# Performance work log

Hardware: AMD Instinct MI355X
Metric: run time of the kernel (lower is better)

The kernel has to match this reference:

```python
import jax, jax.numpy as jnp
import numpy as np

BN_EPS = 1e-5

def _bn_relu(x, gamma, beta):
    # x: [B, C, N]; BatchNorm1d in training mode: stats over (B, N) per channel
    mean = jnp.mean(x, axis=(0, 2), keepdims=True)
    var = jnp.var(x, axis=(0, 2), keepdims=True)
    xn = (x - mean) * jax.lax.rsqrt(var + BN_EPS)
    return jax.nn.relu(xn * gamma[None, :, None] + beta[None, :, None])


def setup_inputs() -> dict:
    key = jax.random.key(0)
    ks = jax.random.split(key, 8)
    B, N, S, D1, D2 = 16, 4096, 1024, 64, 256
    C_in, H = D1 + D2, 256  # mlp_list = [320, 256, 256]
    inp = {
        "xyz1": jax.random.normal(ks[0], (B, 3, N), jnp.float32),
        "xyz2": jax.random.normal(ks[1], (B, 3, S), jnp.float32),
        "points1": jax.random.normal(ks[2], (B, D1, N), jnp.float32),
        "points2": jax.random.normal(ks[3], (B, D2, S), jnp.float32),
        # 1x1 Conv1d weights of the SeqLinear pointNet MLP
        "W1": jax.random.normal(ks[4], (H, C_in), jnp.float32) / np.sqrt(C_in),
        "b1": jnp.zeros((H,), jnp.float32),
        "g1": jnp.ones((H,), jnp.float32),
        "bt1": jnp.zeros((H,), jnp.float32),
        "W2": jax.random.normal(ks[5], (H, H), jnp.float32) / np.sqrt(H),
        "b2": jnp.zeros((H,), jnp.float32),
        "g2": jnp.ones((H,), jnp.float32),
        "bt2": jnp.zeros((H,), jnp.float32),
    }
    return inp


def reference(xyz1, xyz2, points1, points2, W1, b1, g1, bt1, W2, b2, g2, bt2):
    x1 = jnp.transpose(xyz1, (0, 2, 1))   # [B, N, 3]
    x2 = jnp.transpose(xyz2, (0, 2, 1))   # [B, S, 3]
    p2 = jnp.transpose(points2, (0, 2, 1))  # [B, S, D2]
    B, N, _ = x1.shape

    # square_distance: ||x1||^2 + ||x2||^2 - 2 x1.x2  -> [B, N, S]
    dists = (jnp.sum(x1 * x1, axis=-1, keepdims=True)
             + jnp.sum(x2 * x2, axis=-1)[:, None, :]
             - 2.0 * jnp.einsum('bnc,bsc->bns', x1, x2))

    # 3 nearest neighbors (smallest distances)
    neg_d3, idx = jax.lax.top_k(-dists, 3)   # [B, N, 3]
    d3 = -neg_d3
    recip = 1.0 / (d3 + 1e-8)
    weight = recip / jnp.sum(recip, axis=2, keepdims=True)  # [B, N, 3]

    # gather neighbor features: [B, N, 3, D2]
    gathered = jax.vmap(lambda p, i: p[i])(p2, idx)
    interp = jnp.sum(gathered * weight[..., None], axis=2)  # [B, N, D2]

    new_points = jnp.concatenate([jnp.transpose(points1, (0, 2, 1)), interp], axis=-1)
    x = jnp.transpose(new_points, (0, 2, 1))  # [B, 320, N]

    # pointNet MLP: conv1x1 -> BN -> ReLU, twice
    h = jnp.einsum('oc,bcn->bon', W1, x) + b1[None, :, None]
    h = _bn_relu(h, g1, bt1)
    h = jnp.einsum('oc,bcn->bon', W2, h) + b2[None, :, None]
    h = _bn_relu(h, g2, bt2)
    return h
```

## Files before the change

kernel.cpp:

```cpp
#include <hip/hip_runtime.h>
#include <cstddef>

#define B_   16
#define N_   4096
#define S_   1024
#define D1_  64
#define D2_  256
#define CIN_ 320
#define H_   256
#define CH_  8
#define SC_  (S_ / CH_)
#define P_   (B_ * (N_ / 128))

using short8 = __attribute__((ext_vector_type(8))) short;
using f32x4  = __attribute__((ext_vector_type(4))) float;

typedef const __attribute__((address_space(1))) unsigned g1u32;
typedef __attribute__((address_space(3))) unsigned l3u32;

__device__ __forceinline__ void gl_lds16(const void* g, void* l) {
  __builtin_amdgcn_global_load_lds((g1u32*)g, (l3u32*)l, 16, 0, 0);
}

__device__ __forceinline__ float relu_f(float v) { return fmaxf(v, 0.0f); }

__device__ __forceinline__ ushort f2bf(float f) {
  unsigned u = __builtin_bit_cast(unsigned, f);
  u += 0x7fffu + ((u >> 16) & 1u);
  return (ushort)(u >> 16);
}
__device__ __forceinline__ float bf2f(ushort u) {
  return __builtin_bit_cast(float, (unsigned)u << 16);
}

__global__ __launch_bounds__(256) void prep(
    const float* __restrict__ points2, const float* __restrict__ W1,
    const float* __restrict__ W2, ushort* __restrict__ p2tb,
    ushort* __restrict__ W1b, ushort* __restrict__ W2b) {
  int g = blockIdx.x, t = threadIdx.x;
  if (g < 4096) {
    __shared__ float tile[32][33];
    int z = g >> 8, rem = g & 255;
    int c0 = (rem & 31) * 32;
    int r0 = (rem >> 5) * 32;
    const float* in = points2 + (size_t)z * D2_ * S_;
    ushort* out = p2tb + (size_t)z * S_ * D2_;
    int tx = t & 31, ty = t >> 5;
#pragma unroll
    for (int j = 0; j < 4; ++j) {
      int r = r0 + ty + j * 8;
      tile[ty + j * 8][tx] = in[(size_t)r * S_ + c0 + tx];
    }
    __syncthreads();
#pragma unroll
    for (int j = 0; j < 4; ++j) {
      int c = c0 + ty + j * 8;
      out[(size_t)c * D2_ + r0 + tx] = f2bf(tile[tx][ty + j * 8]);
    }
  } else {
    int g2 = g - 4096;
    const float* src = (g2 < 40) ? W1 : W2;
    ushort* dst = (g2 < 40) ? W1b : W2b;
    int base = ((g2 < 40) ? g2 : g2 - 40) * 2048 + t * 8;
    float4 a = *(const float4*)&src[base];
    float4 b = *(const float4*)&src[base + 4];
    short8 r;
    r[0] = (short)f2bf(a.x); r[1] = (short)f2bf(a.y);
    r[2] = (short)f2bf(a.z); r[3] = (short)f2bf(a.w);
    r[4] = (short)f2bf(b.x); r[5] = (short)f2bf(b.y);
    r[6] = (short)f2bf(b.z); r[7] = (short)f2bf(b.w);
    *(short8*)&dst[base] = r;
  }
}

__global__ __launch_bounds__(256) void knn3_part(
    const float* __restrict__ xyz1, const float* __restrict__ xyz2,
    float* __restrict__ pd, int* __restrict__ pi) {
  __shared__ float4 P[SC_];
  int b = blockIdx.z, ch = blockIdx.y;
  int n = blockIdx.x * 256 + threadIdx.x;
  const float* x2b = xyz2 + (size_t)b * 3 * S_ + ch * SC_;
  if (threadIdx.x < SC_) {
    int i = threadIdx.x;
    float x = x2b[i], y = x2b[S_ + i], z = x2b[2 * S_ + i];
    P[i] = make_float4(-2.f * x, -2.f * y, -2.f * z, x * x + y * y + z * z);
  }
  __syncthreads();

  const float* x1b = xyz1 + (size_t)b * 3 * N_;
  float px = x1b[n], py = x1b[N_ + n], pz = x1b[2 * N_ + n];
  float sq1 = px * px + py * py + pz * pz;

  float d0 = 1e30f, d1 = 1e30f, d2 = 1e30f;
  int i0 = 0, i1 = 0, i2 = 0;
#pragma unroll 4
  for (int s = 0; s < SC_; ++s) {
    float4 p = P[s];
    float d = fmaf(px, p.x, fmaf(py, p.y, fmaf(pz, p.z, p.w)));
    int gi = ch * SC_ + s;
    if (d < d2) {
      if (d < d1) {
        if (d < d0) { d2 = d1; i2 = i1; d1 = d0; i1 = i0; d0 = d; i0 = gi; }
        else        { d2 = d1; i2 = i1; d1 = d;  i1 = gi; }
      } else        { d2 = d;  i2 = gi; }
    }
  }
  size_t base = (((size_t)b * N_ + n) * CH_ + ch) * 3;
  pd[base] = d0 + sq1; pd[base + 1] = d1 + sq1; pd[base + 2] = d2 + sq1;
  pi[base] = i0; pi[base + 1] = i1; pi[base + 2] = i2;
}

__global__ __launch_bounds__(256) void build_fused(
    const float* __restrict__ points1,
    const ushort* __restrict__ p2tb,
    const float* __restrict__ pd, const int* __restrict__ pi,
    ushort* __restrict__ xt) {
  __shared__ int   lidx[16][3];
  __shared__ float lw[16][3];
  __shared__ ushort p1t[16][72];
  int g = blockIdx.x, t = threadIdx.x;
  int b = g & 15;
  int p0 = (g >> 4) * 16;

  if (t < 16) {
    size_t pb = (size_t)b * N_ + p0 + t;
    const float* pdp = pd + pb * 24;
    const int*   pip = pi + pb * 24;
    float d0 = 1e30f, d1 = 1e30f, d2 = 1e30f;
    int i0 = 0, i1 = 0, i2 = 0;
#pragma unroll
    for (int k = 0; k < 24; ++k) {
      float d = pdp[k];
      int gi = pip[k];
      if (d < d2) {
        if (d < d1) {
          if (d < d0) { d2 = d1; i2 = i1; d1 = d0; i1 = i0; d0 = d; i0 = gi; }
          else        { d2 = d1; i2 = i1; d1 = d;  i1 = gi; }
        } else        { d2 = d;  i2 = gi; }
      }
    }
    float r0 = 1.0f / (d0 + 1e-8f);
    float r1 = 1.0f / (d1 + 1e-8f);
    float r2 = 1.0f / (d2 + 1e-8f);
    float rs = 1.0f / (r0 + r1 + r2);
    lidx[t][0] = i0; lidx[t][1] = i1; lidx[t][2] = i2;
    lw[t][0] = r0 * rs; lw[t][1] = r1 * rs; lw[t][2] = r2 * rs;
  }

  {
    int c = t >> 2, q4 = t & 3;
    float4 v = *(const float4*)&points1[((size_t)b * D1_ + c) * N_ + p0 + q4 * 4];
    p1t[q4 * 4 + 0][c] = f2bf(v.x);
    p1t[q4 * 4 + 1][c] = f2bf(v.y);
    p1t[q4 * 4 + 2][c] = f2bf(v.z);
    p1t[q4 * 4 + 3][c] = f2bf(v.w);
  }
  __syncthreads();

  int pl = t >> 4, q = t & 15;
  size_t pb = (size_t)b * N_ + p0 + pl;
  int i0 = lidx[pl][0], i1 = lidx[pl][1], i2 = lidx[pl][2];
  float w0 = lw[pl][0], w1 = lw[pl][1], w2 = lw[pl][2];
  const ushort* R0 = p2tb + ((size_t)b * S_ + i0) * D2_;
  const ushort* R1 = p2tb + ((size_t)b * S_ + i1) * D2_;
  const ushort* R2 = p2tb + ((size_t)b * S_ + i2) * D2_;
  ushort* o = xt + pb * CIN_;

  if (q < 8)
    *(short8*)(o + q * 8) = *(const short8*)&p1t[pl][q * 8];

#pragma unroll
  for (int it = 0; it < 2; ++it) {
    int c = it * 16 + q;
    short8 a = *(const short8*)&R0[c * 8];
    short8 d = *(const short8*)&R1[c * 8];
    short8 e = *(const short8*)&R2[c * 8];
    short8 r;
#pragma unroll
    for (int u = 0; u < 8; ++u) {
      float v = w0 * bf2f((ushort)a[u]) + w1 * bf2f((ushort)d[u]) +
                w2 * bf2f((ushort)e[u]);
      r[u] = (short)f2bf(v);
    }
    *(short8*)(o + D1_ + c * 8) = r;
  }
}

template <int K, bool BNIN>
__global__ __launch_bounds__(256) void gemm_pipe(
    const ushort* __restrict__ Wb, const ushort* __restrict__ Xt,
    const float* __restrict__ bias, const float* __restrict__ scin,
    const float* __restrict__ shin, ushort* __restrict__ Yt,
    float* __restrict__ ps1, float* __restrict__ ps2) {
  constexpr int NT = K / 64;
  __shared__ union SM {
    struct { ushort A[2][128][64]; ushort Bt[2][128][64]; } st;
    struct { ushort C[128][132]; float S1[128][33]; float S2[128][33]; } ep;
  } sm;
  __shared__ float scs_l[H_], shs_l[H_];

  int b  = blockIdx.z;
  int n0 = blockIdx.x * 128;
  int m0 = blockIdx.y * 128;
  int tid = threadIdx.x;
  int lane = tid & 63, wid = tid >> 6;
  int wm = (wid >> 1) * 64, wn = (wid & 1) * 64;
  int lr = lane & 15, hi = lane >> 4;
  size_t bn0 = (size_t)b * N_ + n0;

  if (BNIN) {
    for (int i = tid; i < K; i += 256) { scs_l[i] = scin[i]; shs_l[i] = shin[i]; }
  }

  const char* Agb = (const char*)(Wb + (size_t)m0 * K);
  const char* Bgb = (const char*)(Xt + bn0 * K);
  const size_t rowB = (size_t)K * 2;

  size_t gsrc[4];
  int    ldst[4];
#pragma unroll
  for (int r = 0; r < 4; ++r) {
    int m = (wid * 4 + r) * 64 + lane;
    int row = m >> 3;
    int c = ((m & 7) - row) & 7;
    gsrc[r] = (size_t)row * rowB + (size_t)c * 16;
    ldst[r] = m * 16;
  }

  auto stage = [&](int buf, int kc) {
    char* bA = (char*)sm.st.A[buf];
    char* bB = (char*)sm.st.Bt[buf];
    size_t kb = (size_t)kc * 128;
#pragma unroll
    for (int r = 0; r < 4; ++r) {
      gl_lds16(Agb + gsrc[r] + kb, bA + ldst[r]);
      gl_lds16(Bgb + gsrc[r] + kb, bB + ldst[r]);
    }
  };

  f32x4 acc[4][4] = {};

  stage(0, 0);
  __syncthreads();

  int cur = 0;
  for (int t = 0; t < NT; ++t) {
    if (t + 1 < NT) stage(cur ^ 1, t + 1);
#pragma unroll
    for (int ks = 0; ks < 2; ++ks) {
      short8 af[4], bv[4];
#pragma unroll
      for (int i = 0; i < 4; ++i) {
        int rA = wm + i * 16 + lr;
        int rB = wn + i * 16 + lr;
        int sA = (rA + ks * 4 + hi) & 7;
        int sB = (rB + ks * 4 + hi) & 7;
        af[i] = *(const short8*)&sm.st.A[cur][rA][sA * 8];
        bv[i] = *(const short8*)&sm.st.Bt[cur][rB][sB * 8];
      }
      if (BNIN) {
        int kb = t * 64 + ks * 32 + hi * 8;
        f32x4 sa = *(const f32x4*)&scs_l[kb];
        f32x4 sb = *(const f32x4*)&scs_l[kb + 4];
        f32x4 ha = *(const f32x4*)&shs_l[kb];
        f32x4 hb = *(const f32x4*)&shs_l[kb + 4];
#pragma unroll
        for (int i = 0; i < 4; ++i) {
          short8 pk;
#pragma unroll
          for (int e = 0; e < 4; ++e) {
            pk[e]     = (short)f2bf(relu_f(bf2f((ushort)bv[i][e]) * sa[e] + ha[e]));
            pk[e + 4] = (short)f2bf(relu_f(bf2f((ushort)bv[i][e + 4]) * sb[e] + hb[e]));
          }
          bv[i] = pk;
        }
      }
#pragma unroll
      for (int mf = 0; mf < 4; ++mf)
#pragma unroll
        for (int nf = 0; nf < 4; ++nf)
          acc[mf][nf] = __builtin_amdgcn_mfma_f32_16x16x32_bf16(
              af[mf], bv[nf], acc[mf][nf], 0, 0, 0);
    }
    __syncthreads();
    cur ^= 1;
  }

  float sum1[4][4] = {}, sum2[4][4] = {};
#pragma unroll
  for (int mf = 0; mf < 4; ++mf) {
#pragma unroll
    for (int nf = 0; nf < 4; ++nf) {
      int n = wn + nf * 16 + lr;
      ushort4 u;
#pragma unroll
      for (int j = 0; j < 4; ++j) {
        float v = acc[mf][nf][j] + bias[m0 + wm + mf * 16 + hi * 4 + j];
        sum1[mf][j] += v;
        sum2[mf][j] += v * v;
        ((ushort*)&u)[j] = f2bf(v);
      }
      *(ushort4*)&sm.ep.C[n][wm + mf * 16 + hi * 4] = u;
    }
  }
  __syncthreads();
  {
    int rown = tid >> 4, q = tid & 15;
#pragma unroll
    for (int p = 0; p < 8; ++p) {
      int n = p * 16 + rown;
      short8 val = *(const short8*)&sm.ep.C[n][q * 8];
      *(short8*)&Yt[(bn0 + n) * H_ + m0 + q * 8] = val;
    }
  }
  int col = (wid & 1) * 16 + lr;
#pragma unroll
  for (int mf = 0; mf < 4; ++mf)
#pragma unroll
    for (int j = 0; j < 4; ++j) {
      int c = wm + mf * 16 + hi * 4 + j;
      sm.ep.S1[c][col] = sum1[mf][j];
      sm.ep.S2[c][col] = sum2[mf][j];
    }
  __syncthreads();
  int pidx = b * gridDim.x + blockIdx.x;
  int c = tid & 127;
  float s = 0.f;
  if (tid < 128) {
#pragma unroll
    for (int k = 0; k < 32; ++k) s += sm.ep.S1[c][k];
    ps1[(size_t)pidx * H_ + m0 + c] = s;
  } else {
#pragma unroll
    for (int k = 0; k < 32; ++k) s += sm.ep.S2[c][k];
    ps2[(size_t)pidx * H_ + m0 + c] = s;
  }
}

__global__ __launch_bounds__(256) void bn_stats_fin(
    const float* __restrict__ ps1, const float* __restrict__ ps2,
    const float* __restrict__ gamma, const float* __restrict__ beta,
    float* __restrict__ sc, float* __restrict__ sh) {
  int c = blockIdx.x, t = threadIdx.x;
  float s1 = ps1[(size_t)t * H_ + c] + ps1[(size_t)(t + 256) * H_ + c];
  float s2 = ps2[(size_t)t * H_ + c] + ps2[(size_t)(t + 256) * H_ + c];
  __shared__ float S1[256], S2[256];
  S1[t] = s1; S2[t] = s2;
  __syncthreads();
  for (int off = 128; off > 0; off >>= 1) {
    if (t < off) { S1[t] += S1[t + off]; S2[t] += S2[t + off]; }
    __syncthreads();
  }
  if (t == 0) {
    const float inv = 1.0f / (float)(B_ * N_);
    float mean = S1[0] * inv;
    float var  = S2[0] * inv - mean * mean;
    float g    = gamma[c] * rsqrtf(var + 1e-5f);
    sc[c] = g;
    sh[c] = beta[c] - mean * g;
  }
}

__global__ __launch_bounds__(256) void bn_out_t(
    const ushort* __restrict__ Hb, const float* __restrict__ sc,
    const float* __restrict__ sh, float* __restrict__ out) {
  __shared__ float tile[32][132];
  int b = blockIdx.z;
  int n0 = blockIdx.x * 32, m0 = blockIdx.y * 128;
  int t = threadIdx.x;
  int m8 = (t & 15) * 8;
  f32x4 sa = *(const f32x4*)&sc[m0 + m8];
  f32x4 sb = *(const f32x4*)&sc[m0 + m8 + 4];
  f32x4 ha = *(const f32x4*)&sh[m0 + m8];
  f32x4 hb = *(const f32x4*)&sh[m0 + m8 + 4];
  size_t bn0 = (size_t)b * N_ + n0;
#pragma unroll
  for (int pass = 0; pass < 2; ++pass) {
    int n = pass * 16 + (t >> 4);
    short8 v = *(const short8*)&Hb[(bn0 + n) * H_ + m0 + m8];
#pragma unroll
    for (int e = 0; e < 4; ++e) {
      tile[n][m8 + e]     = relu_f(bf2f((ushort)v[e]) * sa[e] + ha[e]);
      tile[n][m8 + 4 + e] = relu_f(bf2f((ushort)v[e + 4]) * sb[e] + hb[e]);
    }
  }
  __syncthreads();
  int m = t >> 1, nh = (t & 1) * 16;
  float* orow = out + ((size_t)b * H_ + m0 + m) * N_ + n0 + nh;
#pragma unroll
  for (int j = 0; j < 4; ++j) {
    float4 v;
    v.x = tile[nh + j * 4 + 0][m];
    v.y = tile[nh + j * 4 + 1][m];
    v.z = tile[nh + j * 4 + 2][m];
    v.w = tile[nh + j * 4 + 3][m];
    *(float4*)&orow[j * 4] = v;
  }
}

extern "C" void kernel_launch(void* const* d_in, const int* in_sizes, int n_in,
                              void* d_out, int out_size, void* d_ws,
                              size_t ws_size, hipStream_t stream) {
  const float* xyz1    = (const float*)d_in[0];
  const float* xyz2    = (const float*)d_in[1];
  const float* points1 = (const float*)d_in[2];
  const float* points2 = (const float*)d_in[3];
  const float* W1  = (const float*)d_in[4];
  const float* b1  = (const float*)d_in[5];
  const float* g1  = (const float*)d_in[6];
  const float* bt1 = (const float*)d_in[7];
  const float* W2  = (const float*)d_in[8];
  const float* b2  = (const float*)d_in[9];
  const float* g2  = (const float*)d_in[10];
  const float* bt2 = (const float*)d_in[11];
  float* out = (float*)d_out;
  char* cur = (char*)d_ws;
  auto alloc = [&](size_t bytes) { char* p = cur; cur += (bytes + 255) & ~255ull; return p; };

  ushort* p2tb = (ushort*)alloc((size_t)B_ * S_ * D2_ * 2);
  float*  pd   = (float*)alloc((size_t)B_ * N_ * CH_ * 3 * 4);
  int*    pi   = (int*)alloc((size_t)B_ * N_ * CH_ * 3 * 4);
  ushort* W1b  = (ushort*)alloc((size_t)H_ * CIN_ * 2);
  ushort* W2b  = (ushort*)alloc((size_t)H_ * H_ * 2);
  ushort* xct  = (ushort*)alloc((size_t)B_ * N_ * CIN_ * 2);
  ushort* h1t  = (ushort*)alloc((size_t)B_ * N_ * H_ * 2);
  float*  ps1  = (float*)alloc((size_t)P_ * H_ * 4);
  float*  ps2  = (float*)alloc((size_t)P_ * H_ * 4);
  float*  sc1  = (float*)alloc(H_ * 4);
  float*  sh1  = (float*)alloc(H_ * 4);
  float*  sc2  = (float*)alloc(H_ * 4);
  float*  sh2  = (float*)alloc(H_ * 4);
  ushort* h2b  = xct;

  prep<<<4096 + 40 + 32, 256, 0, stream>>>(points2, W1, W2, p2tb, W1b, W2b);

  knn3_part<<<dim3(N_ / 256, CH_, B_), 256, 0, stream>>>(xyz1, xyz2, pd, pi);

  build_fused<<<B_ * N_ / 16, 256, 0, stream>>>(points1, p2tb, pd, pi, xct);

  gemm_pipe<CIN_, false><<<dim3(N_ / 128, H_ / 128, B_), 256, 0, stream>>>(
      W1b, xct, b1, nullptr, nullptr, h1t, ps1, ps2);
  bn_stats_fin<<<H_, 256, 0, stream>>>(ps1, ps2, g1, bt1, sc1, sh1);

  gemm_pipe<H_, true><<<dim3(N_ / 128, H_ / 128, B_), 256, 0, stream>>>(
      W2b, h1t, b2, sc1, sh1, h2b, ps1, ps2);
  bn_stats_fin<<<H_, 256, 0, stream>>>(ps1, ps2, g2, bt2, sc2, sh2);

  bn_out_t<<<dim3(N_ / 32, H_ / 128, B_), 256, 0, stream>>>(h2b, sc2, sh2, out);
}
```

Before: 159.5 us.

## Fuse feature interpolation and concat into the first GEMM's B-tile construction

Removes the separate build kernel that wrote the concatenated bf16 input matrix to global memory. The first GEMM now merges the partial KNN results, computes the interpolation weights, loads points1 directly into the first B tile, and builds each later 64-channel B tile from gathered points2 rows while the MFMAs run. This saves a write and re-read of the large intermediate plus one launch. In exchange the interpolation is recomputed once per M-block (two blocks cover H), the B-tile gathers are synchronous per stage, and a separate h2 buffer is now allocated.

New measurement: 166.5 us. +4.4%, slower.

```diff
diff --git a/kernel.cpp b/kernel.cpp
--- a/kernel.cpp
+++ b/kernel.cpp
@@ -110,20 +110,69 @@
   pi[base] = i0; pi[base + 1] = i1; pi[base + 2] = i2;
 }
 
-__global__ __launch_bounds__(256) void build_fused(
+__global__ __launch_bounds__(256) void gemm_build(
+    const ushort* __restrict__ Wb,
     const float* __restrict__ points1,
     const ushort* __restrict__ p2tb,
     const float* __restrict__ pd, const int* __restrict__ pi,
-    ushort* __restrict__ xt) {
-  __shared__ int   lidx[16][3];
-  __shared__ float lw[16][3];
-  __shared__ ushort p1t[16][72];
-  int g = blockIdx.x, t = threadIdx.x;
-  int b = g & 15;
-  int p0 = (g >> 4) * 16;
-
-  if (t < 16) {
-    size_t pb = (size_t)b * N_ + p0 + t;
+    const float* __restrict__ bias, ushort* __restrict__ Yt,
+    float* __restrict__ ps1, float* __restrict__ ps2) {
+  constexpr int K = CIN_, NT = K / 64;
+  __shared__ union SM {
+    struct { ushort A[2][128][64]; ushort Bt[2][128][64]; } st;
+    struct { ushort C[128][132]; float S1[128][33]; float S2[128][33]; } ep;
+  } sm;
+  __shared__ float lw[128][3];
+  __shared__ int   lidx[128][3];
+
+  int b  = blockIdx.z;
+  int n0 = blockIdx.x * 128;
+  int m0 = blockIdx.y * 128;
+  int tid = threadIdx.x;
+  int lane = tid & 63, wid = tid >> 6;
+  int wm = (wid >> 1) * 64, wn = (wid & 1) * 64;
+  int lr = lane & 15, hi = lane >> 4;
+  size_t bn0 = (size_t)b * N_ + n0;
+
+  const char* Agb = (const char*)(Wb + (size_t)m0 * K);
+  const size_t rowB = (size_t)K * 2;
+
+  size_t gsrcA[4];
+  int    ldstA[4];
+#pragma unroll
+  for (int r = 0; r < 4; ++r) {
+    int m = (wid * 4 + r) * 64 + lane;
+    int row = m >> 3;
+    int c = ((m & 7) - row) & 7;
+    gsrcA[r] = (size_t)row * rowB + (size_t)c * 16;
+    ldstA[r] = m * 16;
+  }
+  auto stageA = [&](int buf, int kc) {
+    char* bA = (char*)sm.st.A[buf];
+    size_t kb = (size_t)kc * 128;
+#pragma unroll
+    for (int r = 0; r < 4; ++r)
+      gl_lds16(Agb + gsrcA[r] + kb, bA + ldstA[r]);
+  };
+
+  stageA(0, 0);
+  {
+    int c = tid & 63, nq = tid >> 6;
+    const float* s1 = points1 + ((size_t)b * D1_ + c) * N_ + n0 + nq * 32;
+    int cc0 = c >> 3, ce = c & 7;
+#pragma unroll
+    for (int j = 0; j < 8; ++j) {
+      float4 v = *(const float4*)&s1[j * 4];
+      const float* vp = (const float*)&v;
+#pragma unroll
+      for (int e = 0; e < 4; ++e) {
+        int r = nq * 32 + j * 4 + e;
+        sm.st.Bt[0][r][(((r + cc0) & 7) << 3) + ce] = f2bf(vp[e]);
+      }
+    }
+  }
+  if (tid < 128) {
+    size_t pb = bn0 + tid;
     const float* pdp = pd + pb * 24;
     const int*   pip = pi + pb * 24;
     float d0 = 1e30f, d1 = 1e30f, d2 = 1e30f;
@@ -143,50 +192,117 @@
     float r1 = 1.0f / (d1 + 1e-8f);
     float r2 = 1.0f / (d2 + 1e-8f);
     float rs = 1.0f / (r0 + r1 + r2);
-    lidx[t][0] = i0; lidx[t][1] = i1; lidx[t][2] = i2;
-    lw[t][0] = r0 * rs; lw[t][1] = r1 * rs; lw[t][2] = r2 * rs;
-  }
-
+    lidx[tid][0] = i0; lidx[tid][1] = i1; lidx[tid][2] = i2;
+    lw[tid][0] = r0 * rs; lw[tid][1] = r1 * rs; lw[tid][2] = r2 * rs;
+  }
+  __syncthreads();
+
+  int pt = tid >> 1, hh = (tid & 1) * 4;
+  float w0 = lw[pt][0], w1 = lw[pt][1], w2 = lw[pt][2];
+  const ushort* R0 = p2tb + ((size_t)b * S_ + lidx[pt][0]) * D2_;
+  const ushort* R1 = p2tb + ((size_t)b * S_ + lidx[pt][1]) * D2_;
+  const ushort* R2 = p2tb + ((size_t)b * S_ + lidx[pt][2]) * D2_;
+
+  auto buildB = [&](int buf, int kc) {
+    int pc0 = (kc - 1) * 64;
+#pragma unroll
+    for (int c2 = 0; c2 < 4; ++c2) {
+      int cc = hh + c2;
+      int pch = pc0 + cc * 8;
+      short8 a = *(const short8*)&R0[pch];
+      short8 d = *(const short8*)&R1[pch];
+      short8 e = *(const short8*)&R2[pch];
+      short8 r;
+#pragma unroll
+      for (int u = 0; u < 8; ++u) {
+        float v = w0 * bf2f((ushort)a[u]) + w1 * bf2f((ushort)d[u]) +
+                  w2 * bf2f((ushort)e[u]);
+        r[u] = (short)f2bf(v);
+      }
+      *(short8*)&sm.st.Bt[buf][pt][((pt + cc) & 7) * 8] = r;
+    }
+  };
+
+  f32x4 acc[4][4] = {};
+  int cur = 0;
+  for (int t = 0; t < NT; ++t) {
+    if (t + 1 < NT) stageA(cur ^ 1, t + 1);
+#pragma unroll
+    for (int ks = 0; ks < 2; ++ks) {
+      short8 af[4], bv[4];
+#pragma unroll
+      for (int i = 0; i < 4; ++i) {
+        int rA = wm + i * 16 + lr;
+        int rB = wn + i * 16 + lr;
+        int sA = (rA + ks * 4 + hi) & 7;
+        int sB = (rB + ks * 4 + hi) & 7;
+        af[i] = *(const short8*)&sm.st.A[cur][rA][sA * 8];
+        bv[i] = *(const short8*)&sm.st.Bt[cur][rB][sB * 8];
+      }
+#pragma unroll
+      for (int mf = 0; mf < 4; ++mf)
+#pragma unroll
+        for (int nf = 0; nf < 4; ++nf)
+          acc[mf][nf] = __builtin_amdgcn_mfma_f32_16x16x32_bf16(
+              af[mf], bv[nf], acc[mf][nf], 0, 0, 0);
+    }
+    if (t + 1 < NT) buildB(cur ^ 1, t + 1);
+    __syncthreads();
+    cur ^= 1;
+  }
+
+  float sum1[4][4] = {}, sum2[4][4] = {};
+#pragma unroll
+  for (int mf = 0; mf < 4; ++mf) {
+#pragma unroll
+    for (int nf = 0; nf < 4; ++nf) {
+      int n = wn + nf * 16 + lr;
+      ushort4 u;
+#pragma unroll
+      for (int j = 0; j < 4; ++j) {
+        float v = acc[mf][nf][j] + bias[m0 + wm + mf * 16 + hi * 4 + j];
+        sum1[mf][j] += v;
+        sum2[mf][j] += v * v;
+        ((ushort*)&u)[j] = f2bf(v);
+      }
+      *(ushort4*)&sm.ep.C[n][wm + mf * 16 + hi * 4] = u;
+    }
+  }
+  __syncthreads();
   {
-    int c = t >> 2, q4 = t & 3;
-    float4 v = *(const float4*)&points1[((size_t)b * D1_ + c) * N_ + p0 + q4 * 4];
-    p1t[q4 * 4 + 0][c] = f2bf(v.x);
-    p1t[q4 * 4 + 1][c] = f2bf(v.y);
-    p1t[q4 * 4 + 2][c] = f2bf(v.z);
-    p1t[q4 * 4 + 3][c] = f2bf(v.w);
-  }
-  __syncthreads();
-
-  int pl = t >> 4, q = t & 15;
-  size_t pb = (size_t)b * N_ + p0 + pl;
-  int i0 = lidx[pl][0], i1 = lidx[pl][1], i2 = lidx[pl][2];
-  float w0 = lw[pl][0], w1 = lw[pl][1], w2 = lw[pl][2];
-  const ushort* R0 = p2tb + ((size_t)b * S_ + i0) * D2_;
-  const ushort* R1 = p2tb + ((size_t)b * S_ + i1) * D2_;
-  const ushort* R2 = p2tb + ((size_t)b * S_ + i2) * D2_;
-  ushort* o = xt + pb * CIN_;
-
-  if (q < 8)
-    *(short8*)(o + q * 8) = *(const short8*)&p1t[pl][q * 8];
-
-#pragma unroll
-  for (int it = 0; it < 2; ++it) {
-    int c = it * 16 + q;
-    short8 a = *(const short8*)&R0[c * 8];
-    short8 d = *(const short8*)&R1[c * 8];
-    short8 e = *(const short8*)&R2[c * 8];
-    short8 r;
-#pragma unroll
-    for (int u = 0; u < 8; ++u) {
-      float v = w0 * bf2f((ushort)a[u]) + w1 * bf2f((ushort)d[u]) +
-                w2 * bf2f((ushort)e[u]);
-      r[u] = (short)f2bf(v);
-    }
-    *(short8*)(o + D1_ + c * 8) = r;
-  }
-}
-
-template <int K, bool BNIN>
+    int rown = tid >> 4, q = tid & 15;
+#pragma unroll
+    for (int p = 0; p < 8; ++p) {
+      int n = p * 16 + rown;
+      short8 val = *(const short8*)&sm.ep.C[n][q * 8];
+      *(short8*)&Yt[(bn0 + n) * H_ + m0 + q * 8] = val;
+    }
+  }
+  int col = (wid & 1) * 16 + lr;
+#pragma unroll
+  for (int mf = 0; mf < 4; ++mf)
+#pragma unroll
+    for (int j = 0; j < 4; ++j) {
+      int c = wm + mf * 16 + hi * 4 + j;
+      sm.ep.S1[c][col] = sum1[mf][j];
+      sm.ep.S2[c][col] = sum2[mf][j];
+    }
+  __syncthreads();
+  int pidx = b * gridDim.x + blockIdx.x;
+  int c = tid & 127;
+  float s = 0.f;
+  if (tid < 128) {
+#pragma unroll
+    for (int k = 0; k < 32; ++k) s += sm.ep.S1[c][k];
+    ps1[(size_t)pidx * H_ + m0 + c] = s;
+  } else {
+#pragma unroll
+    for (int k = 0; k < 32; ++k) s += sm.ep.S2[c][k];
+    ps2[(size_t)pidx * H_ + m0 + c] = s;
+  }
+}
+
+template <int K>
 __global__ __launch_bounds__(256) void gemm_pipe(
     const ushort* __restrict__ Wb, const ushort* __restrict__ Xt,
     const float* __restrict__ bias, const float* __restrict__ scin,
@@ -208,9 +324,7 @@
   int lr = lane & 15, hi = lane >> 4;
   size_t bn0 = (size_t)b * N_ + n0;
 
-  if (BNIN) {
-    for (int i = tid; i < K; i += 256) { scs_l[i] = scin[i]; shs_l[i] = shin[i]; }
-  }
+  for (int i = tid; i < K; i += 256) { scs_l[i] = scin[i]; shs_l[i] = shin[i]; }
 
   const char* Agb = (const char*)(Wb + (size_t)m0 * K);
   const char* Bgb = (const char*)(Xt + bn0 * K);
@@ -258,7 +372,7 @@
         af[i] = *(const short8*)&sm.st.A[cur][rA][sA * 8];
         bv[i] = *(const short8*)&sm.st.Bt[cur][rB][sB * 8];
       }
-      if (BNIN) {
+      {
         int kb = t * 64 + ks * 32 + hi * 8;
         f32x4 sa = *(const f32x4*)&scs_l[kb];
         f32x4 sb = *(const f32x4*)&scs_l[kb + 4];
@@ -422,27 +536,24 @@
   int*    pi   = (int*)alloc((size_t)B_ * N_ * CH_ * 3 * 4);
   ushort* W1b  = (ushort*)alloc((size_t)H_ * CIN_ * 2);
   ushort* W2b  = (ushort*)alloc((size_t)H_ * H_ * 2);
-  ushort* xct  = (ushort*)alloc((size_t)B_ * N_ * CIN_ * 2);
   ushort* h1t  = (ushort*)alloc((size_t)B_ * N_ * H_ * 2);
+  ushort* h2b  = (ushort*)alloc((size_t)B_ * N_ * H_ * 2);
   float*  ps1  = (float*)alloc((size_t)P_ * H_ * 4);
   float*  ps2  = (float*)alloc((size_t)P_ * H_ * 4);
   float*  sc1  = (float*)alloc(H_ * 4);
   float*  sh1  = (float*)alloc(H_ * 4);
   float*  sc2  = (float*)alloc(H_ * 4);
   float*  sh2  = (float*)alloc(H_ * 4);
-  ushort* h2b  = xct;
 
   prep<<<4096 + 40 + 32, 256, 0, stream>>>(points2, W1, W2, p2tb, W1b, W2b);
 
   knn3_part<<<dim3(N_ / 256, CH_, B_), 256, 0, stream>>>(xyz1, xyz2, pd, pi);
 
-  build_fused<<<B_ * N_ / 16, 256, 0, stream>>>(points1, p2tb, pd, pi, xct);
-
-  gemm_pipe<CIN_, false><<<dim3(N_ / 128, H_ / 128, B_), 256, 0, stream>>>(
-      W1b, xct, b1, nullptr, nullptr, h1t, ps1, ps2);
+  gemm_build<<<dim3(N_ / 128, H_ / 128, B_), 256, 0, stream>>>(
+      W1b, points1, p2tb, pd, pi, b1, h1t, ps1, ps2);
   bn_stats_fin<<<H_, 256, 0, stream>>>(ps1, ps2, g1, bt1, sc1, sh1);
 
-  gemm_pipe<H_, true><<<dim3(N_ / 128, H_ / 128, B_), 256, 0, stream>>>(
+  gemm_pipe<H_><<<dim3(N_ / 128, H_ / 128, B_), 256, 0, stream>>>(
       W2b, h1t, b2, sc1, sh1, h2b, ps1, ps2);
   bn_stats_fin<<<H_, 256, 0, stream>>>(ps1, ps2, g2, bt2, sc2, sh2);
 
```
